# Performance work log

Measured on AMD Instinct MI355X. Metric: run time of the kernel, lower is better.

The kernel has to match this reference:

```python
import jax, jax.numpy as jnp
import numpy as np

N_NODES = 100000
N_EDGES = 3200000
IN_DIM = 512
OUT_DIM = 256


def setup_inputs() -> dict:
    key = jax.random.key(0)
    k1, k2, k3, k4, k5 = jax.random.split(key, 5)
    features = jax.random.normal(k1, (N_NODES, IN_DIM), dtype=jnp.float32)
    adj_rows = jax.random.randint(k2, (N_EDGES,), 0, N_NODES, dtype=jnp.int32)
    adj_cols = jax.random.randint(k3, (N_EDGES,), 0, N_NODES, dtype=jnp.int32)
    # normalized adjacency values (e.g., 1/sqrt(d_i d_j)); random positive here
    adj_vals = jax.random.uniform(k4, (N_EDGES,), dtype=jnp.float32) * (1.0 / 32.0)
    # xavier uniform for kernel
    limit = np.sqrt(6.0 / (IN_DIM + OUT_DIM)).astype(np.float32)
    kernel = jax.random.uniform(k5, (IN_DIM, OUT_DIM), dtype=jnp.float32, minval=-limit, maxval=limit)
    bias = jnp.zeros((OUT_DIM,), dtype=jnp.float32)
    skip_weight = jnp.ones((OUT_DIM,), dtype=jnp.float32)
    return {
        "features": features,
        "adj_rows": adj_rows,
        "adj_cols": adj_cols,
        "adj_vals": adj_vals,
        "kernel": kernel,
        "bias": bias,
        "skip_weight": skip_weight,
    }


def reference(features, adj_rows, adj_cols, adj_vals, kernel, bias, skip_weight):
    # dense feature transform: [N, in] @ [in, out] -> [N, out]
    xw = jnp.matmul(features, kernel)
    # SpMM: aggregate[i] = sum_e val[e] * xw[col[e]] over edges with row[e] == i
    msgs = adj_vals[:, None] * xw[adj_cols]            # [E, out] gather
    agg = jax.ops.segment_sum(msgs, adj_rows, num_segments=N_NODES)  # [N, out] scatter-add
    out = xw * skip_weight + agg + bias                # skip scale + bias epilogue
    return jax.nn.selu(out)
```

## Files before the change

kernel.cpp:

```cpp
#include <hip/hip_runtime.h>
#include <hip/hip_bf16.h>
#include <cstdint>
#include <cstddef>

#define IN_DIM 512
#define OUT_DIM 256
#define BROWS 256
#define NBUCK_MAX 512

typedef __bf16 bf16x8 __attribute__((ext_vector_type(8)));
typedef float f32x4 __attribute__((ext_vector_type(4)));

__device__ __forceinline__ unsigned short f2bf(float f) {
    __bf16 h = (__bf16)f;
    return __builtin_bit_cast(unsigned short, h);
}
__device__ __forceinline__ float bf2f(unsigned short u) {
    unsigned int x = ((unsigned int)u) << 16;
    return __builtin_bit_cast(float, x);
}
__device__ __forceinline__ float selu(float x) {
    const float kScale = 1.0507009873554805f;
    const float kAlpha = 1.6732632423543772f;
    return (x > 0.f) ? kScale * x : kScale * kAlpha * (expf(x) - 1.f);
}

__global__ void k_convW(const float* __restrict__ W, unsigned short* __restrict__ Wt) {
    int idx = blockIdx.x * 256 + threadIdx.x;
    int n = idx & (OUT_DIM - 1);
    int k = idx >> 8;
    if (k < IN_DIM) Wt[n * IN_DIM + k] = f2bf(W[k * OUT_DIM + n]);
}

__launch_bounds__(512, 2)
__global__ void k_gemm(const float* __restrict__ A, const unsigned short* __restrict__ Wt,
                       signed char* __restrict__ xq, float* __restrict__ scales, int M) {
    __shared__ unsigned short lA[128 * 32];
    __shared__ unsigned short lB[256 * 32];
    __shared__ float lrm[128];
    const int t = threadIdx.x;
    const int wave = t >> 6, lane = t & 63;
    const int wr = wave >> 2, wc = wave & 3;
    const int m0 = blockIdx.x * 128;
    const int mlo = lane & 15, kq = lane >> 4;

    if (t < 128) lrm[t] = 0.f;

    f32x4 acc[4][4] = {};

    for (int k0 = 0; k0 < IN_DIM; k0 += 32) {
        #pragma unroll
        for (int p = 0; p < 2; ++p) {
            int idx = p * 512 + t;
            int r = idx >> 3, c4 = idx & 7;
            int gr = m0 + r; if (gr >= M) gr = M - 1;
            const float4 v = *reinterpret_cast<const float4*>(&A[(size_t)gr * IN_DIM + k0 + c4 * 4]);
            ushort4 u;
            u.x = f2bf(v.x); u.y = f2bf(v.y); u.z = f2bf(v.z); u.w = f2bf(v.w);
            *reinterpret_cast<ushort4*>(&lA[r * 32 + c4 * 4]) = u;
        }
        #pragma unroll
        for (int p = 0; p < 2; ++p) {
            int idx = p * 512 + t;
            int n = idx >> 2, c8 = idx & 3;
            const uint4 v = *reinterpret_cast<const uint4*>(&Wt[(size_t)n * IN_DIM + k0 + c8 * 8]);
            *reinterpret_cast<uint4*>(&lB[n * 32 + c8 * 8]) = v;
        }
        __syncthreads();

        bf16x8 af[4], bfr[4];
        #pragma unroll
        for (int mt = 0; mt < 4; ++mt)
            af[mt] = *reinterpret_cast<const bf16x8*>(&lA[(wr * 64 + mt * 16 + mlo) * 32 + kq * 8]);
        #pragma unroll
        for (int nt = 0; nt < 4; ++nt)
            bfr[nt] = *reinterpret_cast<const bf16x8*>(&lB[(wc * 64 + nt * 16 + mlo) * 32 + kq * 8]);
        #pragma unroll
        for (int mt = 0; mt < 4; ++mt)
            #pragma unroll
            for (int nt = 0; nt < 4; ++nt)
                acc[mt][nt] = __builtin_amdgcn_mfma_f32_16x16x32_bf16(af[mt], bfr[nt], acc[mt][nt], 0, 0, 0);
        __syncthreads();
    }

    #pragma unroll
    for (int mt = 0; mt < 4; ++mt) {
        #pragma unroll
        for (int i = 0; i < 4; ++i) {
            float m = fmaxf(fmaxf(fabsf(acc[mt][0][i]), fabsf(acc[mt][1][i])),
                            fmaxf(fabsf(acc[mt][2][i]), fabsf(acc[mt][3][i])));
            m = fmaxf(m, __shfl_xor(m, 1));
            m = fmaxf(m, __shfl_xor(m, 2));
            m = fmaxf(m, __shfl_xor(m, 4));
            m = fmaxf(m, __shfl_xor(m, 8));
            if (mlo == 0)
                atomicMax(reinterpret_cast<int*>(&lrm[wr * 64 + mt * 16 + kq * 4 + i]),
                          __float_as_int(m));
        }
    }
    __syncthreads();

    #pragma unroll
    for (int mt = 0; mt < 4; ++mt) {
        #pragma unroll
        for (int i = 0; i < 4; ++i) {
            const int rl = wr * 64 + mt * 16 + kq * 4 + i;
            const int row = m0 + rl;
            const float rm = lrm[rl];
            const float inv = (rm > 0.f) ? (127.f / rm) : 0.f;
            if (row < M) {
                #pragma unroll
                for (int nt = 0; nt < 4; ++nt) {
                    int q = (int)rintf(acc[mt][nt][i] * inv);
                    xq[(size_t)row * OUT_DIM + wc * 64 + nt * 16 + mlo] = (signed char)q;
                }
            }
        }
    }
    if (t < 128) {
        int row = m0 + t;
        if (row < M) scales[row] = lrm[t] * (1.f / 127.f);
    }
}

__global__ void k_hist(const int* __restrict__ rows, int* __restrict__ counts, int E) {
    int i = (blockIdx.x * 256 + threadIdx.x) * 4;
    if (i + 4 <= E) {
        int4 r = *reinterpret_cast<const int4*>(&rows[i]);
        atomicAdd(&counts[r.x], 1);
        atomicAdd(&counts[r.y], 1);
        atomicAdd(&counts[r.z], 1);
        atomicAdd(&counts[r.w], 1);
    } else {
        for (int j = i; j < E; ++j) atomicAdd(&counts[rows[j]], 1);
    }
}

__global__ void k_scan1(const int* __restrict__ counts, int* __restrict__ rs,
                        int* __restrict__ bsum, int N) {
    int b = blockIdx.x, t = threadIdx.x;
    int base = b * 1024 + t * 4;
    int4 v = make_int4(0, 0, 0, 0);
    if (base + 4 <= N) v = *reinterpret_cast<const int4*>(&counts[base]);
    else {
        if (base + 0 < N) v.x = counts[base + 0];
        if (base + 1 < N) v.y = counts[base + 1];
        if (base + 2 < N) v.z = counts[base + 2];
        if (base + 3 < N) v.w = counts[base + 3];
    }
    int s0 = v.x, s1 = s0 + v.y, s2 = s1 + v.z, s3 = s2 + v.w;
    __shared__ int sh[256];
    sh[t] = s3; __syncthreads();
    for (int off = 1; off < 256; off <<= 1) {
        int x = (t >= off) ? sh[t - off] : 0;
        __syncthreads();
        sh[t] += x;
        __syncthreads();
    }
    int ex = sh[t] - s3;
    if (base + 0 < N) rs[base + 0] = ex;
    if (base + 1 < N) rs[base + 1] = ex + s0;
    if (base + 2 < N) rs[base + 2] = ex + s1;
    if (base + 3 < N) rs[base + 3] = ex + s2;
    if (t == 255) bsum[b] = sh[255];
}

__global__ void k_scan2(const int* __restrict__ bsum, int* __restrict__ boff, int nb) {
    int t = threadIdx.x;
    __shared__ int sh[256];
    int v = (t < nb) ? bsum[t] : 0;
    sh[t] = v; __syncthreads();
    for (int off = 1; off < 256; off <<= 1) {
        int x = (t >= off) ? sh[t - off] : 0;
        __syncthreads();
        sh[t] += x;
        __syncthreads();
    }
    if (t < nb) boff[t] = sh[t] - v;
}

__global__ void k_scan3(int* __restrict__ rs, int* __restrict__ cursor,
                        const int* __restrict__ boff, int N, int E) {
    int b = blockIdx.x, t = threadIdx.x;
    int base = b * 1024 + t * 4;
    int o = boff[b];
    #pragma unroll
    for (int j = 0; j < 4; ++j) {
        if (base + j < N) {
            int v = rs[base + j] + o;
            rs[base + j] = v;
            cursor[base + j] = v;
        }
    }
    if (b == 0 && t == 0) rs[N] = E;
}

__global__ void k_scatter(const int* __restrict__ rows, const int* __restrict__ cols,
                          const float* __restrict__ vals, const float* __restrict__ scales,
                          int* __restrict__ cursor, int2* __restrict__ ecv, int E) {
    int i = (blockIdx.x * 256 + threadIdx.x) * 4;
    if (i + 4 <= E) {
        int4 r = *reinterpret_cast<const int4*>(&rows[i]);
        int4 c = *reinterpret_cast<const int4*>(&cols[i]);
        float4 v = *reinterpret_cast<const float4*>(&vals[i]);
        int p0 = atomicAdd(&cursor[r.x], 1); ecv[p0] = make_int2(c.x, __float_as_int(v.x * scales[c.x]));
        int p1 = atomicAdd(&cursor[r.y], 1); ecv[p1] = make_int2(c.y, __float_as_int(v.y * scales[c.y]));
        int p2 = atomicAdd(&cursor[r.z], 1); ecv[p2] = make_int2(c.z, __float_as_int(v.z * scales[c.z]));
        int p3 = atomicAdd(&cursor[r.w], 1); ecv[p3] = make_int2(c.w, __float_as_int(v.w * scales[c.w]));
    } else {
        for (int j = i; j < E; ++j) {
            int p = atomicAdd(&cursor[rows[j]], 1);
            ecv[p] = make_int2(cols[j], __float_as_int(vals[j] * scales[cols[j]]));
        }
    }
}

__global__ void k_binit(const int* __restrict__ rs, int* __restrict__ bcursor, int nbuck) {
    int b = blockIdx.x * 256 + threadIdx.x;
    if (b < nbuck) bcursor[b] = rs[b * BROWS];
}

__launch_bounds__(512)
__global__ void k_bin(const int* __restrict__ rows, const int* __restrict__ cols,
                      const float* __restrict__ vals, int* __restrict__ bcursor,
                      int2* __restrict__ binned, int E) {
    __shared__ int cnt[NBUCK_MAX];
    __shared__ int scn[NBUCK_MAX];
    __shared__ int dlt[NBUCK_MAX];
    const int t = threadIdx.x;
    const int base = blockIdx.x * 8192;

    cnt[t] = 0;
    __syncthreads();

    int er[16], ec[16];
    float ev[16];
    #pragma unroll
    for (int p = 0; p < 4; ++p) {
        const int i = base + p * 2048 + (t << 2);
        if (i + 4 <= E) {
            int4 r4 = *reinterpret_cast<const int4*>(&rows[i]);
            int4 c4 = *reinterpret_cast<const int4*>(&cols[i]);
            float4 v4 = *reinterpret_cast<const float4*>(&vals[i]);
            er[4*p+0] = r4.x; ec[4*p+0] = c4.x; ev[4*p+0] = v4.x;
            er[4*p+1] = r4.y; ec[4*p+1] = c4.y; ev[4*p+1] = v4.y;
            er[4*p+2] = r4.z; ec[4*p+2] = c4.z; ev[4*p+2] = v4.z;
            er[4*p+3] = r4.w; ec[4*p+3] = c4.w; ev[4*p+3] = v4.w;
        } else {
            #pragma unroll
            for (int j = 0; j < 4; ++j) {
                int idx = i + j;
                bool ok = idx < E;
                er[4*p+j] = ok ? rows[idx] : -1;
                ec[4*p+j] = ok ? cols[idx] : 0;
                ev[4*p+j] = ok ? vals[idx] : 0.f;
            }
        }
    }

    #pragma unroll
    for (int k = 0; k < 16; ++k)
        if (er[k] >= 0) atomicAdd(&cnt[er[k] >> 8], 1);
    __syncthreads();

    int v = cnt[t];
    scn[t] = v;
    __syncthreads();
    for (int off = 1; off < NBUCK_MAX; off <<= 1) {
        int x = (t >= off) ? scn[t - off] : 0;
        __syncthreads();
        scn[t] += x;
        __syncthreads();
    }
    int ex = scn[t] - v;

    int d = 0;
    if (v > 0) d = atomicAdd(&bcursor[t], v) - ex;
    dlt[t] = d;
    cnt[t] = ex;
    __syncthreads();

    #pragma unroll
    for (int k = 0; k < 16; ++k) {
        if (er[k] >= 0) {
            int b = er[k] >> 8;
            int lp = atomicAdd(&cnt[b], 1);
            binned[(size_t)(dlt[b] + lp)] =
                make_int2(ec[k] | ((er[k] & 255) << 17), __float_as_int(ev[k]));
        }
    }
}

__launch_bounds__(256)
__global__ void k_fine(const int2* __restrict__ binned, const int* __restrict__ rs,
                       const float* __restrict__ scales, int2* __restrict__ ecv, int M) {
    __shared__ int lcur[BROWS];
    const int b = blockIdx.x, t = threadIdx.x;
    const int r0 = b * BROWS;
    const int rend = min(r0 + BROWS, M);
    if (r0 + t < rend) lcur[t] = rs[r0 + t];
    const int start = __builtin_amdgcn_readfirstlane(rs[r0]);
    const int end   = __builtin_amdgcn_readfirstlane(rs[rend]);
    __syncthreads();
    for (int i = start + t; i < end; i += 256) {
        int2 rec = binned[i];
        int r = rec.x >> 17;
        int col = rec.x & 0x1FFFF;
        int pos = atomicAdd(&lcur[r], 1);
        ecv[pos] = make_int2(col, __float_as_int(__int_as_float(rec.y) * scales[col]));
    }
}

__launch_bounds__(256)
__global__ void k_agg(const signed char* __restrict__ xq,
                      const float* __restrict__ scales,
                      const int2* __restrict__ ecv,
                      const int* __restrict__ rs,
                      const float* __restrict__ skipw,
                      const float* __restrict__ bias,
                      float* __restrict__ out, int M) {
    const int wave = threadIdx.x >> 6, lane = threadIdx.x & 63;
    const int node = blockIdx.x * 4 + wave;
    if (node >= M) return;
    const int s = __builtin_amdgcn_readfirstlane(rs[node]);
    const int e = __builtin_amdgcn_readfirstlane(rs[node + 1]);
    const int d4 = lane * 4;

    float a0 = 0.f, a1 = 0.f, a2 = 0.f, a3 = 0.f;
    int p = s;
    constexpr int U = 8;
    for (; p + U <= e; p += U) {
        int   cs[U];
        float vs[U];
        #pragma unroll
        for (int u = 0; u < U; ++u) {
            int2 c = ecv[p + u];
            cs[u] = c.x; vs[u] = __int_as_float(c.y);
        }
        int g[U];
        #pragma unroll
        for (int u = 0; u < U; ++u)
            g[u] = *reinterpret_cast<const int*>(&xq[(size_t)cs[u] * OUT_DIM + d4]);
        #pragma unroll
        for (int u = 0; u < U; ++u) {
            a0 += vs[u] * (float)(signed char)(g[u]);
            a1 += vs[u] * (float)(signed char)(g[u] >> 8);
            a2 += vs[u] * (float)(signed char)(g[u] >> 16);
            a3 += vs[u] * (float)(g[u] >> 24);
        }
    }
    for (; p < e; ++p) {
        int2 c = ecv[p];
        float v = __int_as_float(c.y);
        int g = *reinterpret_cast<const int*>(&xq[(size_t)c.x * OUT_DIM + d4]);
        a0 += v * (float)(signed char)(g);
        a1 += v * (float)(signed char)(g >> 8);
        a2 += v * (float)(signed char)(g >> 16);
        a3 += v * (float)(g >> 24);
    }

    int w = *reinterpret_cast<const int*>(&xq[(size_t)node * OUT_DIM + d4]);
    float sc = scales[node];
    float x0 = (float)(signed char)(w)        * sc;
    float x1 = (float)(signed char)(w >> 8)   * sc;
    float x2 = (float)(signed char)(w >> 16)  * sc;
    float x3 = (float)(w >> 24)               * sc;

    float4 sw = *reinterpret_cast<const float4*>(&skipw[d4]);
    float4 bi = *reinterpret_cast<const float4*>(&bias[d4]);
    float4 r;
    r.x = selu(a0 + x0 * sw.x + bi.x);
    r.y = selu(a1 + x1 * sw.y + bi.y);
    r.z = selu(a2 + x2 * sw.z + bi.z);
    r.w = selu(a3 + x3 * sw.w + bi.w);
    *reinterpret_cast<float4*>(&out[(size_t)node * OUT_DIM + d4]) = r;
}

extern "C" void kernel_launch(void* const* d_in, const int* in_sizes, int n_in,
                              void* d_out, int out_size, void* d_ws, size_t ws_size,
                              hipStream_t stream) {
    const float* features = (const float*)d_in[0];
    const int*   adj_rows = (const int*)d_in[1];
    const int*   adj_cols = (const int*)d_in[2];
    const float* adj_vals = (const float*)d_in[3];
    const float* Wk       = (const float*)d_in[4];
    const float* bias     = (const float*)d_in[5];
    const float* skipw    = (const float*)d_in[6];
    float* out = (float*)d_out;

    const int M = in_sizes[0] / IN_DIM;
    const int E = in_sizes[1];

    char* w = (char*)d_ws;
    size_t off = 0;
    auto carve = [&](size_t bytes) -> void* {
        void* p = w + off;
        off = (off + bytes + 255) & ~(size_t)255;
        return p;
    };
    signed char* xq = (signed char*)carve((size_t)M * OUT_DIM);
    float* scales   = (float*)carve((size_t)M * 4);
    unsigned short* Wt = (unsigned short*)carve((size_t)IN_DIM * OUT_DIM * 2);
    int*  counts = (int*)carve((size_t)M * 4);
    int*  rs     = (int*)carve((size_t)(M + 1) * 4);
    int*  cursor = (int*)carve((size_t)M * 4);
    int*  bsum   = (int*)carve(256 * 4);
    int*  boff   = (int*)carve(256 * 4);
    int*  bcur   = (int*)carve(NBUCK_MAX * 4);
    int2* ecv    = (int2*)carve((size_t)E * 8);
    int2* binned = (int2*)carve((size_t)E * 8);
    const int nbuck = (M + BROWS - 1) / BROWS;
    const bool use_binned = (off <= ws_size) && (nbuck <= NBUCK_MAX) && (M <= (1 << 17));

    hipMemsetAsync(counts, 0, (size_t)M * 4, stream);

    k_convW<<<(IN_DIM * OUT_DIM + 255) / 256, 256, 0, stream>>>(Wk, Wt);
    k_gemm<<<(M + 127) / 128, 512, 0, stream>>>(features, Wt, xq, scales, M);

    k_hist<<<(E / 4 + 255) / 256, 256, 0, stream>>>(adj_rows, counts, E);
    int nb = (M + 1023) / 1024;
    k_scan1<<<nb, 256, 0, stream>>>(counts, rs, bsum, M);
    k_scan2<<<1, 256, 0, stream>>>(bsum, boff, nb);
    k_scan3<<<nb, 256, 0, stream>>>(rs, cursor, boff, M, E);

    if (use_binned) {
        k_binit<<<(nbuck + 255) / 256, 256, 0, stream>>>(rs, bcur, nbuck);
        k_bin<<<(E + 8191) / 8192, 512, 0, stream>>>(adj_rows, adj_cols, adj_vals, bcur, binned, E);
        k_fine<<<nbuck, 256, 0, stream>>>(binned, rs, scales, ecv, M);
    } else {
        k_scatter<<<(E / 4 + 255) / 256, 256, 0, stream>>>(adj_rows, adj_cols, adj_vals, scales, cursor, ecv, E);
    }

    k_agg<<<(M + 3) / 4, 256, 0, stream>>>(xq, scales, ecv, rs, skipw, bias, out, M);
}
```

Baseline: 674.7 us.

## Replace per-row global histogram and scans with bucket-level histogram and in-block row offsets

The binned path no longer builds a global per-row histogram with atomics and three scan kernels. Instead it counts edges per 256-row bucket in shared memory, scans the bucket counts in one block, and computes per-row offsets inside the fine-sort kernel from a local shared histogram of the already-binned edges. This removes a memset over M ints, millions of global atomics, and several small kernel launches. In exchange the fine kernel reads the binned data twice.

```diff
diff --git a/kernel.cpp b/kernel.cpp
--- a/kernel.cpp
+++ b/kernel.cpp
@@ -123,101 +123,48 @@
     }
 }
 
-__global__ void k_hist(const int* __restrict__ rows, int* __restrict__ counts, int E) {
-    int i = (blockIdx.x * 256 + threadIdx.x) * 4;
-    if (i + 4 <= E) {
-        int4 r = *reinterpret_cast<const int4*>(&rows[i]);
-        atomicAdd(&counts[r.x], 1);
-        atomicAdd(&counts[r.y], 1);
-        atomicAdd(&counts[r.z], 1);
-        atomicAdd(&counts[r.w], 1);
-    } else {
-        for (int j = i; j < E; ++j) atomicAdd(&counts[rows[j]], 1);
-    }
-}
-
-__global__ void k_scan1(const int* __restrict__ counts, int* __restrict__ rs,
-                        int* __restrict__ bsum, int N) {
-    int b = blockIdx.x, t = threadIdx.x;
-    int base = b * 1024 + t * 4;
-    int4 v = make_int4(0, 0, 0, 0);
-    if (base + 4 <= N) v = *reinterpret_cast<const int4*>(&counts[base]);
-    else {
-        if (base + 0 < N) v.x = counts[base + 0];
-        if (base + 1 < N) v.y = counts[base + 1];
-        if (base + 2 < N) v.z = counts[base + 2];
-        if (base + 3 < N) v.w = counts[base + 3];
-    }
-    int s0 = v.x, s1 = s0 + v.y, s2 = s1 + v.z, s3 = s2 + v.w;
-    __shared__ int sh[256];
-    sh[t] = s3; __syncthreads();
-    for (int off = 1; off < 256; off <<= 1) {
+__launch_bounds__(512)
+__global__ void k_bhist(const int* __restrict__ rows, int* __restrict__ bcnt, int E) {
+    __shared__ int cnt[NBUCK_MAX];
+    const int t = threadIdx.x;
+    const int base = blockIdx.x * 8192;
+    cnt[t] = 0;
+    __syncthreads();
+    #pragma unroll
+    for (int p = 0; p < 4; ++p) {
+        const int i = base + p * 2048 + (t << 2);
+        if (i + 4 <= E) {
+            int4 r4 = *reinterpret_cast<const int4*>(&rows[i]);
+            atomicAdd(&cnt[r4.x >> 8], 1);
+            atomicAdd(&cnt[r4.y >> 8], 1);
+            atomicAdd(&cnt[r4.z >> 8], 1);
+            atomicAdd(&cnt[r4.w >> 8], 1);
+        } else if (i < E) {
+            for (int j = i; j < E && j < i + 4; ++j) atomicAdd(&cnt[rows[j] >> 8], 1);
+        }
+    }
+    __syncthreads();
+    if (cnt[t] > 0) atomicAdd(&bcnt[t], cnt[t]);
+}
+
+__launch_bounds__(NBUCK_MAX)
+__global__ void k_bscan(const int* __restrict__ bcnt, int* __restrict__ bbase,
+                        int* __restrict__ bcursor, int nbuck, int E) {
+    const int t = threadIdx.x;
+    __shared__ int sh[NBUCK_MAX];
+    int v = (t < nbuck) ? bcnt[t] : 0;
+    sh[t] = v;
+    __syncthreads();
+    for (int off = 1; off < NBUCK_MAX; off <<= 1) {
         int x = (t >= off) ? sh[t - off] : 0;
         __syncthreads();
         sh[t] += x;
         __syncthreads();
     }
-    int ex = sh[t] - s3;
-    if (base + 0 < N) rs[base + 0] = ex;
-    if (base + 1 < N) rs[base + 1] = ex + s0;
-    if (base + 2 < N) rs[base + 2] = ex + s1;
-    if (base + 3 < N) rs[base + 3] = ex + s2;
-    if (t == 255) bsum[b] = sh[255];
-}
-
-__global__ void k_scan2(const int* __restrict__ bsum, int* __restrict__ boff, int nb) {
-    int t = threadIdx.x;
-    __shared__ int sh[256];
-    int v = (t < nb) ? bsum[t] : 0;
-    sh[t] = v; __syncthreads();
-    for (int off = 1; off < 256; off <<= 1) {
-        int x = (t >= off) ? sh[t - off] : 0;
-        __syncthreads();
-        sh[t] += x;
-        __syncthreads();
-    }
-    if (t < nb) boff[t] = sh[t] - v;
-}
-
-__global__ void k_scan3(int* __restrict__ rs, int* __restrict__ cursor,
-                        const int* __restrict__ boff, int N, int E) {
-    int b = blockIdx.x, t = threadIdx.x;
-    int base = b * 1024 + t * 4;
-    int o = boff[b];
-    #pragma unroll
-    for (int j = 0; j < 4; ++j) {
-        if (base + j < N) {
-            int v = rs[base + j] + o;
-            rs[base + j] = v;
-            cursor[base + j] = v;
-        }
-    }
-    if (b == 0 && t == 0) rs[N] = E;
-}
-
-__global__ void k_scatter(const int* __restrict__ rows, const int* __restrict__ cols,
-                          const float* __restrict__ vals, const float* __restrict__ scales,
-                          int* __restrict__ cursor, int2* __restrict__ ecv, int E) {
-    int i = (blockIdx.x * 256 + threadIdx.x) * 4;
-    if (i + 4 <= E) {
-        int4 r = *reinterpret_cast<const int4*>(&rows[i]);
-        int4 c = *reinterpret_cast<const int4*>(&cols[i]);
-        float4 v = *reinterpret_cast<const float4*>(&vals[i]);
-        int p0 = atomicAdd(&cursor[r.x], 1); ecv[p0] = make_int2(c.x, __float_as_int(v.x * scales[c.x]));
-        int p1 = atomicAdd(&cursor[r.y], 1); ecv[p1] = make_int2(c.y, __float_as_int(v.y * scales[c.y]));
-        int p2 = atomicAdd(&cursor[r.z], 1); ecv[p2] = make_int2(c.z, __float_as_int(v.z * scales[c.z]));
-        int p3 = atomicAdd(&cursor[r.w], 1); ecv[p3] = make_int2(c.w, __float_as_int(v.w * scales[c.w]));
-    } else {
-        for (int j = i; j < E; ++j) {
-            int p = atomicAdd(&cursor[rows[j]], 1);
-            ecv[p] = make_int2(cols[j], __float_as_int(vals[j] * scales[cols[j]]));
-        }
-    }
-}
-
-__global__ void k_binit(const int* __restrict__ rs, int* __restrict__ bcursor, int nbuck) {
-    int b = blockIdx.x * 256 + threadIdx.x;
-    if (b < nbuck) bcursor[b] = rs[b * BROWS];
+    int ex = sh[t] - v;
+    bbase[t] = ex;
+    bcursor[t] = ex;
+    if (t == 0) bbase[NBUCK_MAX] = E;
 }
 
 __launch_bounds__(512)
@@ -292,22 +239,135 @@
 }
 
 __launch_bounds__(256)
-__global__ void k_fine(const int2* __restrict__ binned, const int* __restrict__ rs,
-                       const float* __restrict__ scales, int2* __restrict__ ecv, int M) {
+__global__ void k_fine2(const int2* __restrict__ binned, const int* __restrict__ bbase,
+                        const float* __restrict__ scales, int2* __restrict__ ecv,
+                        int* __restrict__ rs, int M, int E, int nbuck) {
+    __shared__ int lcnt[BROWS];
     __shared__ int lcur[BROWS];
     const int b = blockIdx.x, t = threadIdx.x;
     const int r0 = b * BROWS;
-    const int rend = min(r0 + BROWS, M);
-    if (r0 + t < rend) lcur[t] = rs[r0 + t];
-    const int start = __builtin_amdgcn_readfirstlane(rs[r0]);
-    const int end   = __builtin_amdgcn_readfirstlane(rs[rend]);
-    __syncthreads();
+    lcnt[t] = 0;
+    const int start = __builtin_amdgcn_readfirstlane(bbase[b]);
+    const int end   = __builtin_amdgcn_readfirstlane(bbase[b + 1]);
+    __syncthreads();
+
+    for (int i = start + t; i < end; i += 256)
+        atomicAdd(&lcnt[binned[i].x >> 17], 1);
+    __syncthreads();
+
+    int v = lcnt[t];
+    lcur[t] = v;
+    __syncthreads();
+    for (int off = 1; off < 256; off <<= 1) {
+        int x = (t >= off) ? lcur[t - off] : 0;
+        __syncthreads();
+        lcur[t] += x;
+        __syncthreads();
+    }
+    int rowoff = start + (lcur[t] - v);
+    if (r0 + t < M) rs[r0 + t] = rowoff;
+    if (b == nbuck - 1 && t == 0) rs[M] = E;
+    lcur[t] = rowoff;
+    __syncthreads();
+
     for (int i = start + t; i < end; i += 256) {
         int2 rec = binned[i];
         int r = rec.x >> 17;
         int col = rec.x & 0x1FFFF;
         int pos = atomicAdd(&lcur[r], 1);
         ecv[pos] = make_int2(col, __float_as_int(__int_as_float(rec.y) * scales[col]));
+    }
+}
+
+__global__ void k_hist(const int* __restrict__ rows, int* __restrict__ counts, int E) {
+    int i = (blockIdx.x * 256 + threadIdx.x) * 4;
+    if (i + 4 <= E) {
+        int4 r = *reinterpret_cast<const int4*>(&rows[i]);
+        atomicAdd(&counts[r.x], 1);
+        atomicAdd(&counts[r.y], 1);
+        atomicAdd(&counts[r.z], 1);
+        atomicAdd(&counts[r.w], 1);
+    } else {
+        for (int j = i; j < E; ++j) atomicAdd(&counts[rows[j]], 1);
+    }
+}
+
+__global__ void k_scan1(const int* __restrict__ counts, int* __restrict__ rs,
+                        int* __restrict__ bsum, int N) {
+    int b = blockIdx.x, t = threadIdx.x;
+    int base = b * 1024 + t * 4;
+    int4 v = make_int4(0, 0, 0, 0);
+    if (base + 4 <= N) v = *reinterpret_cast<const int4*>(&counts[base]);
+    else {
+        if (base + 0 < N) v.x = counts[base + 0];
+        if (base + 1 < N) v.y = counts[base + 1];
+        if (base + 2 < N) v.z = counts[base + 2];
+        if (base + 3 < N) v.w = counts[base + 3];
+    }
+    int s0 = v.x, s1 = s0 + v.y, s2 = s1 + v.z, s3 = s2 + v.w;
+    __shared__ int sh[256];
+    sh[t] = s3; __syncthreads();
+    for (int off = 1; off < 256; off <<= 1) {
+        int x = (t >= off) ? sh[t - off] : 0;
+        __syncthreads();
+        sh[t] += x;
+        __syncthreads();
+    }
+    int ex = sh[t] - s3;
+    if (base + 0 < N) rs[base + 0] = ex;
+    if (base + 1 < N) rs[base + 1] = ex + s0;
+    if (base + 2 < N) rs[base + 2] = ex + s1;
+    if (base + 3 < N) rs[base + 3] = ex + s2;
+    if (t == 255) bsum[b] = sh[255];
+}
+
+__global__ void k_scan2(const int* __restrict__ bsum, int* __restrict__ boff, int nb) {
+    int t = threadIdx.x;
+    __shared__ int sh[256];
+    int v = (t < nb) ? bsum[t] : 0;
+    sh[t] = v; __syncthreads();
+    for (int off = 1; off < 256; off <<= 1) {
+        int x = (t >= off) ? sh[t - off] : 0;
+        __syncthreads();
+        sh[t] += x;
+        __syncthreads();
+    }
+    if (t < nb) boff[t] = sh[t] - v;
+}
+
+__global__ void k_scan3(int* __restrict__ rs, int* __restrict__ cursor,
+                        const int* __restrict__ boff, int N, int E) {
+    int b = blockIdx.x, t = threadIdx.x;
+    int base = b * 1024 + t * 4;
+    int o = boff[b];
+    #pragma unroll
+    for (int j = 0; j < 4; ++j) {
+        if (base + j < N) {
+            int v = rs[base + j] + o;
+            rs[base + j] = v;
+            cursor[base + j] = v;
+        }
+    }
+    if (b == 0 && t == 0) rs[N] = E;
+}
+
+__global__ void k_scatter(const int* __restrict__ rows, const int* __restrict__ cols,
+                          const float* __restrict__ vals, const float* __restrict__ scales,
+                          int* __restrict__ cursor, int2* __restrict__ ecv, int E) {
+    int i = (blockIdx.x * 256 + threadIdx.x) * 4;
+    if (i + 4 <= E) {
+        int4 r = *reinterpret_cast<const int4*>(&rows[i]);
+        int4 c = *reinterpret_cast<const int4*>(&cols[i]);
+        float4 v = *reinterpret_cast<const float4*>(&vals[i]);
+        int p0 = atomicAdd(&cursor[r.x], 1); ecv[p0] = make_int2(c.x, __float_as_int(v.x * scales[c.x]));
+        int p1 = atomicAdd(&cursor[r.y], 1); ecv[p1] = make_int2(c.y, __float_as_int(v.y * scales[c.y]));
+        int p2 = atomicAdd(&cursor[r.z], 1); ecv[p2] = make_int2(c.z, __float_as_int(v.z * scales[c.z]));
+        int p3 = atomicAdd(&cursor[r.w], 1); ecv[p3] = make_int2(c.w, __float_as_int(v.w * scales[c.w]));
+    } else {
+        for (int j = i; j < E; ++j) {
+            int p = atomicAdd(&cursor[rows[j]], 1);
+            ecv[p] = make_int2(cols[j], __float_as_int(vals[j] * scales[cols[j]]));
+        }
     }
 }
 
@@ -406,28 +466,30 @@
     int*  cursor = (int*)carve((size_t)M * 4);
     int*  bsum   = (int*)carve(256 * 4);
     int*  boff   = (int*)carve(256 * 4);
-    int*  bcur   = (int*)carve(NBUCK_MAX * 4);
+    int*  bcnt   = (int*)carve((NBUCK_MAX + 1) * 4);
+    int*  bbase  = (int*)carve((NBUCK_MAX + 1) * 4);
+    int*  bcur   = (int*)carve((NBUCK_MAX + 1) * 4);
     int2* ecv    = (int2*)carve((size_t)E * 8);
     int2* binned = (int2*)carve((size_t)E * 8);
     const int nbuck = (M + BROWS - 1) / BROWS;
     const bool use_binned = (off <= ws_size) && (nbuck <= NBUCK_MAX) && (M <= (1 << 17));
 
-    hipMemsetAsync(counts, 0, (size_t)M * 4, stream);
-
     k_convW<<<(IN_DIM * OUT_DIM + 255) / 256, 256, 0, stream>>>(Wk, Wt);
     k_gemm<<<(M + 127) / 128, 512, 0, stream>>>(features, Wt, xq, scales, M);
 
-    k_hist<<<(E / 4 + 255) / 256, 256, 0, stream>>>(adj_rows, counts, E);
-    int nb = (M + 1023) / 1024;
-    k_scan1<<<nb, 256, 0, stream>>>(counts, rs, bsum, M);
-    k_scan2<<<1, 256, 0, stream>>>(bsum, boff, nb);
-    k_scan3<<<nb, 256, 0, stream>>>(rs, cursor, boff, M, E);
-
     if (use_binned) {
-        k_binit<<<(nbuck + 255) / 256, 256, 0, stream>>>(rs, bcur, nbuck);
+        hipMemsetAsync(bcnt, 0, (NBUCK_MAX + 1) * 4, stream);
+        k_bhist<<<(E + 8191) / 8192, 512, 0, stream>>>(adj_rows, bcnt, E);
+        k_bscan<<<1, NBUCK_MAX, 0, stream>>>(bcnt, bbase, bcur, nbuck, E);
         k_bin<<<(E + 8191) / 8192, 512, 0, stream>>>(adj_rows, adj_cols, adj_vals, bcur, binned, E);
-        k_fine<<<nbuck, 256, 0, stream>>>(binned, rs, scales, ecv, M);
+        k_fine2<<<nbuck, 256, 0, stream>>>(binned, bbase, scales, ecv, rs, M, E, nbuck);
     } else {
+        hipMemsetAsync(counts, 0, (size_t)M * 4, stream);
+        k_hist<<<(E / 4 + 255) / 256, 256, 0, stream>>>(adj_rows, counts, E);
+        int nb = (M + 1023) / 1024;
+        k_scan1<<<nb, 256, 0, stream>>>(counts, rs, bsum, M);
+        k_scan2<<<1, 256, 0, stream>>>(bsum, boff, nb);
+        k_scan3<<<nb, 256, 0, stream>>>(rs, cursor, boff, M, E);
         k_scatter<<<(E / 4 + 255) / 256, 256, 0, stream>>>(adj_rows, adj_cols, adj_vals, scales, cursor, ecv, E);
     }
 
```

After: 567.0 us. 1.19x faster.
